# Kernel tuning notes

Measured on AMD Instinct MI355X. Metric: run time of the kernel, lower is better.

The kernel has to match this reference:

```python
import jax, jax.numpy as jnp
import numpy as np

EPS = 1e-12
SIMILARITY = 'dot'  # non-tensor forward arg, closed over


def setup_inputs() -> dict:
    key = jax.random.key(0)
    k1, k2, k3, k4 = jax.random.split(key, 4)
    N, M, D = 4096, 8192, 512
    x = jax.random.normal(k1, (N, D), dtype=jnp.float32)
    x_n = jax.random.normal(k2, (M, D), dtype=jnp.float32)
    # Linear(D, 3) params
    W = jax.random.normal(k3, (3, D), dtype=jnp.float32) * (1.0 / np.sqrt(D))
    bias = jax.random.normal(k4, (3,), dtype=jnp.float32) * 0.01
    return {"x": x, "x_n": x_n, "W": W, "bias": bias}


def _sim_matrix(x, x_n, similarity):
    if similarity == 'l2':
        d2 = (jnp.sum(x * x, 1)[:, None] - 2.0 * (x @ x_n.T)
              + jnp.sum(x_n * x_n, 1)[None, :])
        return -jnp.sqrt(jnp.maximum(d2, 0.0))
    elif similarity == 'l1':
        return -jnp.sum(jnp.abs(x[:, None, :] - x_n[None, :, :]), axis=-1)
    elif similarity == 'dot':
        return (x @ x_n.T) / x.shape[1]
    elif similarity == 'cos':
        xn = x / jnp.linalg.norm(x, axis=1, keepdims=True)
        yn = x_n / jnp.linalg.norm(x_n, axis=1, keepdims=True)
        return xn @ yn.T


def reference(x, x_n, W, bias):
    # pointwise params from a Linear(D,3)+Sigmoid head, clamped to (eps, 1-eps)
    p = jnp.clip(jax.nn.sigmoid(x @ W.T + bias), EPS, 1.0 - EPS)  # [N,3]
    a = p[:, 0:1]
    b = p[:, 1:2]
    s = p[:, 2:3]
    b = a + b * (1.0 - a)

    sim = _sim_matrix(x, x_n, SIMILARITY)                # [N,M]
    smin = jnp.min(sim, axis=1, keepdims=True)
    smax = jnp.max(sim, axis=1, keepdims=True)
    sim_norm = (sim - smin) / (smax - smin)

    # x != x_n -> plain row max (torch.equal branch is False)
    top_sims = jnp.max(sim_norm, axis=1, keepdims=True)  # [N,1]
    a = jnp.minimum(a, top_sims) - EPS

    num = jnp.maximum(jnp.abs(sim_norm - a) ** (1.0 / s), EPS)
    denom = num + jnp.maximum(jnp.abs(b - sim_norm) ** (1.0 / s), EPS)
    soft_mask = num / denom

    lo = sim_norm < a
    hi = sim_norm > b
    soft_mask = jnp.where(lo, 0.0, jnp.where(hi, 1.0, soft_mask))
    # safe log: masked-to-0 entries give -inf forward, zero grad (matches torch)
    safe = jnp.where(lo, 1.0, soft_mask)
    log_mask = jnp.where(lo, -jnp.inf, jnp.log(safe))
    return sim + log_mask
```

## Files before the change

### kernel.cpp

```cpp
#include <hip/hip_runtime.h>
#include <hip/hip_fp16.h>
#include <math.h>

#define EPSF 1e-12f
#define NEG_HUGE (-1e30f)

typedef _Float16 half8_t __attribute__((ext_vector_type(8)));
typedef _Float16 half4_t __attribute__((ext_vector_type(4)));
typedef float floatx4 __attribute__((ext_vector_type(4)));

__device__ __forceinline__ float sigmoid_stable(float v) {
    if (v >= 0.0f) {
        return 1.0f / (1.0f + expf(-v));
    } else {
        float e = expf(v);
        return e / (1.0f + e);
    }
}

__global__ __launch_bounds__(64) void row_params_kernel(
    const float* __restrict__ x, const float* __restrict__ W,
    const float* __restrict__ bias,
    float* __restrict__ aeff, float* __restrict__ bnew, float* __restrict__ tinv)
{
    const int r = blockIdx.x;
    const int l = threadIdx.x;
    const float* xr = x + (size_t)r * 512;
    float s0 = 0.0f, s1 = 0.0f, s2 = 0.0f;
#pragma unroll
    for (int i = 0; i < 8; ++i) {
        int e = l * 8 + i;
        float xv = xr[e];
        s0 = fmaf(xv, W[e], s0);
        s1 = fmaf(xv, W[512 + e], s1);
        s2 = fmaf(xv, W[1024 + e], s2);
    }
#pragma unroll
    for (int off = 32; off > 0; off >>= 1) {
        s0 += __shfl_xor(s0, off);
        s1 += __shfl_xor(s1, off);
        s2 += __shfl_xor(s2, off);
    }
    if (l == 0) {
        float p0 = fminf(fmaxf(sigmoid_stable(s0 + bias[0]), EPSF), 1.0f);
        float p1 = fminf(fmaxf(sigmoid_stable(s1 + bias[1]), EPSF), 1.0f);
        float p2 = fminf(fmaxf(sigmoid_stable(s2 + bias[2]), EPSF), 1.0f);
        float b = p0 + p1 * (1.0f - p0);
        float ae = fminf(p0, 1.0f) - EPSF;
        aeff[r] = ae;
        bnew[r] = b;
        tinv[r] = 1.0f / p2;
    }
}

__global__ __launch_bounds__(256) void split_fp32_f16_kernel(
    const float* __restrict__ src, _Float16* __restrict__ dst,
    int seg_lo, int nrows)
{
    int idx = blockIdx.x * 256 + threadIdx.x;
    int row = idx >> 7;
    int c = (idx & 127) << 2;
    if (row >= nrows) return;
    float4 v = *(const float4*)(src + (size_t)row * 512 + c);
    _Float16 h0 = (_Float16)v.x, h1 = (_Float16)v.y,
             h2 = (_Float16)v.z, h3 = (_Float16)v.w;
    half4_t hv = {h0, h1, h2, h3};
    half4_t lv = {(_Float16)(v.x - (float)h0), (_Float16)(v.y - (float)h1),
                  (_Float16)(v.z - (float)h2), (_Float16)(v.w - (float)h3)};
    _Float16* d = dst + (size_t)row * 1536 + c;
    *(half4_t*)(d) = hv;
    *(half4_t*)(d + 512)  = (seg_lo == 1) ? lv : hv;
    *(half4_t*)(d + 1024) = (seg_lo == 1) ? hv : lv;
}

__device__ __forceinline__ void load_tile_row16(
    const _Float16* gbase, _Float16* lds_base, int lane)
{
    const _Float16* g = gbase + (size_t)(lane >> 2) * 1536 + (size_t)(lane & 3) * 8;
    __builtin_amdgcn_global_load_lds(
        (const __attribute__((address_space(1))) unsigned int*)g,
        (__attribute__((address_space(3))) unsigned int*)lds_base,
        16, 0, 0);
}

__global__ __launch_bounds__(256) void mfma_gemm_kernel(
    const _Float16* __restrict__ A, const _Float16* __restrict__ B,
    float* __restrict__ C)
{
    constexpr int Kp = 1536;
    constexpr int N = 8192;
    __shared__ __align__(16) _Float16 As[128 * 32];
    __shared__ __align__(16) _Float16 Bs[128 * 32];

    const int t = threadIdx.x;
    const int wave = t >> 6;
    const int lane = t & 63;
    const int bx = blockIdx.x;
    const int by = blockIdx.y;

    const _Float16* Abase = A + (size_t)(by * 128 + wave * 16) * Kp;
    const _Float16* Bbase = B + (size_t)(bx * 128 + wave * 16) * Kp;
    _Float16* AsW0 = &As[(wave * 16) * 32];
    _Float16* AsW1 = &As[(64 + wave * 16) * 32];
    _Float16* BsW0 = &Bs[(wave * 16) * 32];
    _Float16* BsW1 = &Bs[(64 + wave * 16) * 32];
    const size_t rs64 = (size_t)64 * Kp;

    const int wm = (wave >> 1) * 64;
    const int wn = (wave & 1) * 64;
    const _Float16* aptr = &As[(wm + (lane & 15)) * 32 + (lane >> 4) * 8];
    const _Float16* bptr = &Bs[(wn + (lane & 15)) * 32 + (lane >> 4) * 8];

    floatx4 acc[4][4] = {};

    for (int kt = 0; kt < Kp / 32; ++kt) {
        const _Float16* Ak = Abase + kt * 32;
        const _Float16* Bk = Bbase + kt * 32;
        load_tile_row16(Ak, AsW0, lane);
        load_tile_row16(Ak + rs64, AsW1, lane);
        load_tile_row16(Bk, BsW0, lane);
        load_tile_row16(Bk + rs64, BsW1, lane);
        __syncthreads();

        half8_t af[4], bf[4];
#pragma unroll
        for (int i = 0; i < 4; ++i) af[i] = *(const half8_t*)(aptr + i * 16 * 32);
#pragma unroll
        for (int j = 0; j < 4; ++j) bf[j] = *(const half8_t*)(bptr + j * 16 * 32);
#pragma unroll
        for (int i = 0; i < 4; ++i)
#pragma unroll
            for (int j = 0; j < 4; ++j)
                acc[i][j] = __builtin_amdgcn_mfma_f32_16x16x32_f16(
                    af[i], bf[j], acc[i][j], 0, 0, 0);
        __syncthreads();
    }

    const float sc = 1.0f / 512.0f;
    const int row0 = by * 128 + wm + (lane >> 4) * 4;
    const int col0 = bx * 128 + wn + (lane & 15);
#pragma unroll
    for (int i = 0; i < 4; ++i) {
#pragma unroll
        for (int r = 0; r < 4; ++r) {
            float* cp = C + (size_t)(row0 + i * 16 + r) * N + col0;
#pragma unroll
            for (int j = 0; j < 4; ++j)
                cp[j * 16] = acc[i][j][r] * sc;
        }
    }
}

#define BM 128
#define BN 128
#define BK 16
__global__ __launch_bounds__(256) void sgemm_nt_kernel(
    const float* __restrict__ A, const float* __restrict__ B,
    float* __restrict__ C)
{
    const int K = 512;
    const int N = 8192;
    __shared__ float As[BK][BM];
    __shared__ float Bs[BK][BN];
    const int t = threadIdx.x;
    const int bx = blockIdx.x, by = blockIdx.y;
    const int m0 = t >> 2;
    const int kq = (t & 3) << 2;
    const float* Ap = A + ((size_t)(by * BM + m0) * K + kq);
    const float* Bp = B + ((size_t)(bx * BN + m0) * K + kq);
    const int tx = t & 15, ty = t >> 4;
    float acc[8][8] = {};
    float4 a0 = *(const float4*)(Ap), a1 = *(const float4*)(Ap + (size_t)64 * K);
    float4 b0 = *(const float4*)(Bp), b1 = *(const float4*)(Bp + (size_t)64 * K);
    for (int kt = 0; kt < K / BK; ++kt) {
        As[kq + 0][m0] = a0.x; As[kq + 1][m0] = a0.y; As[kq + 2][m0] = a0.z; As[kq + 3][m0] = a0.w;
        As[kq + 0][m0 + 64] = a1.x; As[kq + 1][m0 + 64] = a1.y; As[kq + 2][m0 + 64] = a1.z; As[kq + 3][m0 + 64] = a1.w;
        Bs[kq + 0][m0] = b0.x; Bs[kq + 1][m0] = b0.y; Bs[kq + 2][m0] = b0.z; Bs[kq + 3][m0] = b0.w;
        Bs[kq + 0][m0 + 64] = b1.x; Bs[kq + 1][m0 + 64] = b1.y; Bs[kq + 2][m0 + 64] = b1.z; Bs[kq + 3][m0 + 64] = b1.w;
        __syncthreads();
        if (kt + 1 < K / BK) {
            const float* Ap2 = Ap + (size_t)(kt + 1) * BK;
            const float* Bp2 = Bp + (size_t)(kt + 1) * BK;
            a0 = *(const float4*)(Ap2); a1 = *(const float4*)(Ap2 + (size_t)64 * K);
            b0 = *(const float4*)(Bp2); b1 = *(const float4*)(Bp2 + (size_t)64 * K);
        }
#pragma unroll
        for (int k = 0; k < BK; ++k) {
            float4 xa0 = *(const float4*)(&As[k][ty * 8]);
            float4 xa1 = *(const float4*)(&As[k][ty * 8 + 4]);
            float4 yb0 = *(const float4*)(&Bs[k][tx * 8]);
            float4 yb1 = *(const float4*)(&Bs[k][tx * 8 + 4]);
            float av[8] = {xa0.x, xa0.y, xa0.z, xa0.w, xa1.x, xa1.y, xa1.z, xa1.w};
            float bv[8] = {yb0.x, yb0.y, yb0.z, yb0.w, yb1.x, yb1.y, yb1.z, yb1.w};
#pragma unroll
            for (int i = 0; i < 8; ++i)
#pragma unroll
                for (int j = 0; j < 8; ++j)
                    acc[i][j] = fmaf(av[i], bv[j], acc[i][j]);
        }
        __syncthreads();
    }
    const float sc = 1.0f / 512.0f;
    const int gm = by * BM + ty * 8, gn = bx * BN + tx * 8;
#pragma unroll
    for (int i = 0; i < 8; ++i) {
        float4 o0 = make_float4(acc[i][0] * sc, acc[i][1] * sc, acc[i][2] * sc, acc[i][3] * sc);
        float4 o1 = make_float4(acc[i][4] * sc, acc[i][5] * sc, acc[i][6] * sc, acc[i][7] * sc);
        float* cp = C + (size_t)(gm + i) * N + gn;
        *(float4*)(cp) = o0;
        *(float4*)(cp + 4) = o1;
    }
}

__global__ __launch_bounds__(256) void row_minmax_kernel(
    const float* __restrict__ C, float* __restrict__ smin, float* __restrict__ smax)
{
    const int r = blockIdx.x;
    const float4* row = (const float4*)(C + (size_t)r * 8192);
    float mn = INFINITY, mx = -INFINITY;
#pragma unroll
    for (int i = 0; i < 8; ++i) {
        float4 v = row[threadIdx.x + i * 256];
        mn = fminf(mn, fminf(fminf(v.x, v.y), fminf(v.z, v.w)));
        mx = fmaxf(mx, fmaxf(fmaxf(v.x, v.y), fmaxf(v.z, v.w)));
    }
#pragma unroll
    for (int off = 32; off > 0; off >>= 1) {
        mn = fminf(mn, __shfl_xor(mn, off));
        mx = fmaxf(mx, __shfl_xor(mx, off));
    }
    __shared__ float smn[4], smx[4];
    if ((threadIdx.x & 63) == 0) {
        smn[threadIdx.x >> 6] = mn;
        smx[threadIdx.x >> 6] = mx;
    }
    __syncthreads();
    if (threadIdx.x == 0) {
        mn = fminf(fminf(smn[0], smn[1]), fminf(smn[2], smn[3]));
        mx = fmaxf(fmaxf(smx[0], smx[1]), fmaxf(smx[2], smx[3]));
        smin[r] = mn;
        smax[r] = mx;
    }
}

__device__ __forceinline__ float fast_pow(float x, float t) {
    return __expf(t * __logf(x));
}

__global__ __launch_bounds__(256) void epilogue_kernel(
    float* __restrict__ C,
    const float* __restrict__ aeff, const float* __restrict__ bnew,
    const float* __restrict__ tinv,
    const float* __restrict__ smin, const float* __restrict__ smax)
{
    const int r = blockIdx.y;
    const int c4 = blockIdx.x * 256 + threadIdx.x;
    const float a = aeff[r];
    const float b = bnew[r];
    const float t = tinv[r];
    const float mn = smin[r];
    const float range = smax[r] - mn;
    const float inv_range = (range > 0.0f) ? (1.0f / range) : 0.0f;

    float4* p = (float4*)(C + (size_t)r * 8192) + c4;
    float4 v = *p;
    float sv[4] = {v.x, v.y, v.z, v.w};
    float out[4];
#pragma unroll
    for (int i = 0; i < 4; ++i) {
        float sim = sv[i];
        float sn = (sim - mn) * inv_range;
        float lm;
        if (sn < a) {
            lm = NEG_HUGE;
        } else if (sn > b) {
            lm = 0.0f;
        } else {
            float num = fmaxf(fast_pow(fabsf(sn - a), t), EPSF);
            float den = num + fmaxf(fast_pow(fabsf(b - sn), t), EPSF);
            lm = __logf(num / den);
        }
        out[i] = sim + lm;
    }
    *p = make_float4(out[0], out[1], out[2], out[3]);
}

extern "C" void kernel_launch(void* const* d_in, const int* in_sizes, int n_in,
                              void* d_out, int out_size, void* d_ws, size_t ws_size,
                              hipStream_t stream)
{
    const float* x    = (const float*)d_in[0];
    const float* x_n  = (const float*)d_in[1];
    const float* W    = (const float*)d_in[2];
    const float* bias = (const float*)d_in[3];
    float* C = (float*)d_out;
    float* ws = (float*)d_ws;

    float* aeff = ws;
    float* bnew = ws + 4096;
    float* tinv = ws + 8192;
    float* smin = ws + 12288;
    float* smax = ws + 16384;

    const size_t a2_off = 128 * 1024;
    const size_t a2_bytes = (size_t)4096 * 1536 * 2;
    const size_t b2_off = a2_off + a2_bytes;
    const size_t need = b2_off + (size_t)8192 * 1536 * 2;

    row_params_kernel<<<4096, 64, 0, stream>>>(x, W, bias, aeff, bnew, tinv);

    if (ws_size >= need) {
        _Float16* A2 = (_Float16*)((char*)d_ws + a2_off);
        _Float16* B2 = (_Float16*)((char*)d_ws + b2_off);
        split_fp32_f16_kernel<<<2048, 256, 0, stream>>>(x, A2, 2, 4096);
        split_fp32_f16_kernel<<<4096, 256, 0, stream>>>(x_n, B2, 1, 8192);
        mfma_gemm_kernel<<<dim3(64, 32), 256, 0, stream>>>(A2, B2, C);
    } else {
        sgemm_nt_kernel<<<dim3(8192 / BN, 4096 / BM), 256, 0, stream>>>(x, x_n, C);
    }

    row_minmax_kernel<<<4096, 256, 0, stream>>>(C, smin, smax);
    epilogue_kernel<<<dim3(8192 / 4 / 256, 4096), 256, 0, stream>>>(C, aeff, bnew, tinv, smin, smax);
}
```

Baseline: 336.3 us.

## Fuse row min/max into GEMM epilogue via ordered-int atomics; merge split kernels

The separate row min/max pass over the 128MB similarity matrix is removed. Each GEMM block instead reduces its tile's per-row min and max with shuffles, then updates global ordered-uint encodings using atomicMin and atomicMax, which row_params_kernel initializes. The two fp16 split kernels become one launch, the epilogue uses nontemporal loads and stores, and the fp32 SGEMM fallback is dropped, so the workspace is assumed large enough. This saves a full read of C and two launches, at the cost of atomic contention and extra epilogue work inside the GEMM.

```diff
diff --git a/kernel.cpp b/kernel.cpp
--- a/kernel.cpp
+++ b/kernel.cpp
@@ -18,10 +18,20 @@
     }
 }
 
+__device__ __forceinline__ unsigned enc_ord(float f) {
+    unsigned u = __float_as_uint(f);
+    return (u & 0x80000000u) ? ~u : (u | 0x80000000u);
+}
+__device__ __forceinline__ float dec_ord(unsigned e) {
+    unsigned u = (e & 0x80000000u) ? (e & 0x7fffffffu) : ~e;
+    return __uint_as_float(u);
+}
+
 __global__ __launch_bounds__(64) void row_params_kernel(
     const float* __restrict__ x, const float* __restrict__ W,
     const float* __restrict__ bias,
-    float* __restrict__ aeff, float* __restrict__ bnew, float* __restrict__ tinv)
+    float* __restrict__ aeff, float* __restrict__ bnew, float* __restrict__ tinv,
+    unsigned* __restrict__ encMin, unsigned* __restrict__ encMax)
 {
     const int r = blockIdx.x;
     const int l = threadIdx.x;
@@ -50,27 +60,40 @@
         aeff[r] = ae;
         bnew[r] = b;
         tinv[r] = 1.0f / p2;
-    }
-}
-
-__global__ __launch_bounds__(256) void split_fp32_f16_kernel(
-    const float* __restrict__ src, _Float16* __restrict__ dst,
-    int seg_lo, int nrows)
+        encMin[r] = 0xFFFFFFFFu;
+        encMax[r] = 0u;
+    }
+}
+
+__global__ __launch_bounds__(256) void split_both_kernel(
+    const float* __restrict__ x, const float* __restrict__ xn,
+    _Float16* __restrict__ A2, _Float16* __restrict__ B2)
 {
     int idx = blockIdx.x * 256 + threadIdx.x;
     int row = idx >> 7;
     int c = (idx & 127) << 2;
-    if (row >= nrows) return;
-    float4 v = *(const float4*)(src + (size_t)row * 512 + c);
+    const float* src;
+    _Float16* dst;
+    bool isB;
+    if (row < 4096) {
+        src = x + (size_t)row * 512 + c;
+        dst = A2 + (size_t)row * 1536 + c;
+        isB = false;
+    } else {
+        int r = row - 4096;
+        src = xn + (size_t)r * 512 + c;
+        dst = B2 + (size_t)r * 1536 + c;
+        isB = true;
+    }
+    float4 v = *(const float4*)src;
     _Float16 h0 = (_Float16)v.x, h1 = (_Float16)v.y,
              h2 = (_Float16)v.z, h3 = (_Float16)v.w;
     half4_t hv = {h0, h1, h2, h3};
     half4_t lv = {(_Float16)(v.x - (float)h0), (_Float16)(v.y - (float)h1),
                   (_Float16)(v.z - (float)h2), (_Float16)(v.w - (float)h3)};
-    _Float16* d = dst + (size_t)row * 1536 + c;
-    *(half4_t*)(d) = hv;
-    *(half4_t*)(d + 512)  = (seg_lo == 1) ? lv : hv;
-    *(half4_t*)(d + 1024) = (seg_lo == 1) ? hv : lv;
+    *(half4_t*)(dst) = hv;
+    *(half4_t*)(dst + 512)  = isB ? lv : hv;
+    *(half4_t*)(dst + 1024) = isB ? hv : lv;
 }
 
 __device__ __forceinline__ void load_tile_row16(
@@ -85,7 +108,8 @@
 
 __global__ __launch_bounds__(256) void mfma_gemm_kernel(
     const _Float16* __restrict__ A, const _Float16* __restrict__ B,
-    float* __restrict__ C)
+    float* __restrict__ C,
+    unsigned* __restrict__ encMin, unsigned* __restrict__ encMax)
 {
     constexpr int Kp = 1536;
     constexpr int N = 8192;
@@ -149,97 +173,37 @@
                 cp[j * 16] = acc[i][j][r] * sc;
         }
     }
-}
-
-#define BM 128
-#define BN 128
-#define BK 16
-__global__ __launch_bounds__(256) void sgemm_nt_kernel(
-    const float* __restrict__ A, const float* __restrict__ B,
-    float* __restrict__ C)
-{
-    const int K = 512;
-    const int N = 8192;
-    __shared__ float As[BK][BM];
-    __shared__ float Bs[BK][BN];
-    const int t = threadIdx.x;
-    const int bx = blockIdx.x, by = blockIdx.y;
-    const int m0 = t >> 2;
-    const int kq = (t & 3) << 2;
-    const float* Ap = A + ((size_t)(by * BM + m0) * K + kq);
-    const float* Bp = B + ((size_t)(bx * BN + m0) * K + kq);
-    const int tx = t & 15, ty = t >> 4;
-    float acc[8][8] = {};
-    float4 a0 = *(const float4*)(Ap), a1 = *(const float4*)(Ap + (size_t)64 * K);
-    float4 b0 = *(const float4*)(Bp), b1 = *(const float4*)(Bp + (size_t)64 * K);
-    for (int kt = 0; kt < K / BK; ++kt) {
-        As[kq + 0][m0] = a0.x; As[kq + 1][m0] = a0.y; As[kq + 2][m0] = a0.z; As[kq + 3][m0] = a0.w;
-        As[kq + 0][m0 + 64] = a1.x; As[kq + 1][m0 + 64] = a1.y; As[kq + 2][m0 + 64] = a1.z; As[kq + 3][m0 + 64] = a1.w;
-        Bs[kq + 0][m0] = b0.x; Bs[kq + 1][m0] = b0.y; Bs[kq + 2][m0] = b0.z; Bs[kq + 3][m0] = b0.w;
-        Bs[kq + 0][m0 + 64] = b1.x; Bs[kq + 1][m0 + 64] = b1.y; Bs[kq + 2][m0 + 64] = b1.z; Bs[kq + 3][m0 + 64] = b1.w;
-        __syncthreads();
-        if (kt + 1 < K / BK) {
-            const float* Ap2 = Ap + (size_t)(kt + 1) * BK;
-            const float* Bp2 = Bp + (size_t)(kt + 1) * BK;
-            a0 = *(const float4*)(Ap2); a1 = *(const float4*)(Ap2 + (size_t)64 * K);
-            b0 = *(const float4*)(Bp2); b1 = *(const float4*)(Bp2 + (size_t)64 * K);
+
+    float mnv[4][4], mxv[4][4];
+#pragma unroll
+    for (int i = 0; i < 4; ++i)
+#pragma unroll
+        for (int r = 0; r < 4; ++r) {
+            float lo = fminf(fminf(acc[i][0][r], acc[i][1][r]),
+                             fminf(acc[i][2][r], acc[i][3][r]));
+            float hi = fmaxf(fmaxf(acc[i][0][r], acc[i][1][r]),
+                             fmaxf(acc[i][2][r], acc[i][3][r]));
+            mnv[i][r] = lo * sc;
+            mxv[i][r] = hi * sc;
         }
 #pragma unroll
-        for (int k = 0; k < BK; ++k) {
-            float4 xa0 = *(const float4*)(&As[k][ty * 8]);
-            float4 xa1 = *(const float4*)(&As[k][ty * 8 + 4]);
-            float4 yb0 = *(const float4*)(&Bs[k][tx * 8]);
-            float4 yb1 = *(const float4*)(&Bs[k][tx * 8 + 4]);
-            float av[8] = {xa0.x, xa0.y, xa0.z, xa0.w, xa1.x, xa1.y, xa1.z, xa1.w};
-            float bv[8] = {yb0.x, yb0.y, yb0.z, yb0.w, yb1.x, yb1.y, yb1.z, yb1.w};
-#pragma unroll
-            for (int i = 0; i < 8; ++i)
-#pragma unroll
-                for (int j = 0; j < 8; ++j)
-                    acc[i][j] = fmaf(av[i], bv[j], acc[i][j]);
-        }
-        __syncthreads();
-    }
-    const float sc = 1.0f / 512.0f;
-    const int gm = by * BM + ty * 8, gn = bx * BN + tx * 8;
-#pragma unroll
-    for (int i = 0; i < 8; ++i) {
-        float4 o0 = make_float4(acc[i][0] * sc, acc[i][1] * sc, acc[i][2] * sc, acc[i][3] * sc);
-        float4 o1 = make_float4(acc[i][4] * sc, acc[i][5] * sc, acc[i][6] * sc, acc[i][7] * sc);
-        float* cp = C + (size_t)(gm + i) * N + gn;
-        *(float4*)(cp) = o0;
-        *(float4*)(cp + 4) = o1;
-    }
-}
-
-__global__ __launch_bounds__(256) void row_minmax_kernel(
-    const float* __restrict__ C, float* __restrict__ smin, float* __restrict__ smax)
-{
-    const int r = blockIdx.x;
-    const float4* row = (const float4*)(C + (size_t)r * 8192);
-    float mn = INFINITY, mx = -INFINITY;
-#pragma unroll
-    for (int i = 0; i < 8; ++i) {
-        float4 v = row[threadIdx.x + i * 256];
-        mn = fminf(mn, fminf(fminf(v.x, v.y), fminf(v.z, v.w)));
-        mx = fmaxf(mx, fmaxf(fmaxf(v.x, v.y), fmaxf(v.z, v.w)));
-    }
-#pragma unroll
-    for (int off = 32; off > 0; off >>= 1) {
-        mn = fminf(mn, __shfl_xor(mn, off));
-        mx = fmaxf(mx, __shfl_xor(mx, off));
-    }
-    __shared__ float smn[4], smx[4];
-    if ((threadIdx.x & 63) == 0) {
-        smn[threadIdx.x >> 6] = mn;
-        smx[threadIdx.x >> 6] = mx;
-    }
-    __syncthreads();
-    if (threadIdx.x == 0) {
-        mn = fminf(fminf(smn[0], smn[1]), fminf(smn[2], smn[3]));
-        mx = fmaxf(fmaxf(smx[0], smx[1]), fmaxf(smx[2], smx[3]));
-        smin[r] = mn;
-        smax[r] = mx;
+    for (int off = 1; off < 16; off <<= 1)
+#pragma unroll
+        for (int i = 0; i < 4; ++i)
+#pragma unroll
+            for (int r = 0; r < 4; ++r) {
+                mnv[i][r] = fminf(mnv[i][r], __shfl_xor(mnv[i][r], off));
+                mxv[i][r] = fmaxf(mxv[i][r], __shfl_xor(mxv[i][r], off));
+            }
+    if ((lane & 15) == 0) {
+#pragma unroll
+        for (int i = 0; i < 4; ++i)
+#pragma unroll
+            for (int r = 0; r < 4; ++r) {
+                int row = row0 + i * 16 + r;
+                atomicMin(&encMin[row], enc_ord(mnv[i][r]));
+                atomicMax(&encMax[row], enc_ord(mxv[i][r]));
+            }
     }
 }
 
@@ -251,24 +215,23 @@
     float* __restrict__ C,
     const float* __restrict__ aeff, const float* __restrict__ bnew,
     const float* __restrict__ tinv,
-    const float* __restrict__ smin, const float* __restrict__ smax)
+    const unsigned* __restrict__ encMin, const unsigned* __restrict__ encMax)
 {
     const int r = blockIdx.y;
     const int c4 = blockIdx.x * 256 + threadIdx.x;
     const float a = aeff[r];
     const float b = bnew[r];
     const float t = tinv[r];
-    const float mn = smin[r];
-    const float range = smax[r] - mn;
+    const float mn = dec_ord(encMin[r]);
+    const float range = dec_ord(encMax[r]) - mn;
     const float inv_range = (range > 0.0f) ? (1.0f / range) : 0.0f;
 
-    float4* p = (float4*)(C + (size_t)r * 8192) + c4;
-    float4 v = *p;
-    float sv[4] = {v.x, v.y, v.z, v.w};
-    float out[4];
+    floatx4* p = (floatx4*)(C + (size_t)r * 8192) + c4;
+    floatx4 v = __builtin_nontemporal_load(p);
+    floatx4 out;
 #pragma unroll
     for (int i = 0; i < 4; ++i) {
-        float sim = sv[i];
+        float sim = v[i];
         float sn = (sim - mn) * inv_range;
         float lm;
         if (sn < a) {
@@ -282,7 +245,7 @@
         }
         out[i] = sim + lm;
     }
-    *p = make_float4(out[0], out[1], out[2], out[3]);
+    __builtin_nontemporal_store(out, p);
 }
 
 extern "C" void kernel_launch(void* const* d_in, const int* in_sizes, int n_in,
@@ -299,26 +262,19 @@
     float* aeff = ws;
     float* bnew = ws + 4096;
     float* tinv = ws + 8192;
-    float* smin = ws + 12288;
-    float* smax = ws + 16384;
+    unsigned* encMin = (unsigned*)(ws + 12288);
+    unsigned* encMax = (unsigned*)(ws + 16384);
 
     const size_t a2_off = 128 * 1024;
     const size_t a2_bytes = (size_t)4096 * 1536 * 2;
     const size_t b2_off = a2_off + a2_bytes;
-    const size_t need = b2_off + (size_t)8192 * 1536 * 2;
-
-    row_params_kernel<<<4096, 64, 0, stream>>>(x, W, bias, aeff, bnew, tinv);
-
-    if (ws_size >= need) {
-        _Float16* A2 = (_Float16*)((char*)d_ws + a2_off);
-        _Float16* B2 = (_Float16*)((char*)d_ws + b2_off);
-        split_fp32_f16_kernel<<<2048, 256, 0, stream>>>(x, A2, 2, 4096);
-        split_fp32_f16_kernel<<<4096, 256, 0, stream>>>(x_n, B2, 1, 8192);
-        mfma_gemm_kernel<<<dim3(64, 32), 256, 0, stream>>>(A2, B2, C);
-    } else {
-        sgemm_nt_kernel<<<dim3(8192 / BN, 4096 / BM), 256, 0, stream>>>(x, x_n, C);
-    }
-
-    row_minmax_kernel<<<4096, 256, 0, stream>>>(C, smin, smax);
-    epilogue_kernel<<<dim3(8192 / 4 / 256, 4096), 256, 0, stream>>>(C, aeff, bnew, tinv, smin, smax);
-}
+    _Float16* A2 = (_Float16*)((char*)d_ws + a2_off);
+    _Float16* B2 = (_Float16*)((char*)d_ws + b2_off);
+
+    row_params_kernel<<<4096, 64, 0, stream>>>(x, W, bias, aeff, bnew, tinv,
+                                               encMin, encMax);
+    split_both_kernel<<<6144, 256, 0, stream>>>(x, x_n, A2, B2);
+    mfma_gemm_kernel<<<dim3(64, 32), 256, 0, stream>>>(A2, B2, C, encMin, encMax);
+    epilogue_kernel<<<dim3(8, 4096), 256, 0, stream>>>(C, aeff, bnew, tinv,
+                                                       encMin, encMax);
+}
```

New measurement: 342.0 us. No clear change (+1.7%).

## Fuse row min/max partials into MFMA GEMM epilogue and merge split kernels

Applied to the files above, without the earlier changes.

The GEMM epilogue now computes per-row min/max partials over each wave's 64-column slice and writes them to a workspace buffer. A small reduction kernel combines them, which removes the full-matrix row_minmax pass that re-read the 128MB similarity matrix. The two fp16 split kernels are merged into a single launch, and the epilogue uses nontemporal loads and stores. The cost is extra shuffle work and partial-buffer writes inside the GEMM, plus a larger workspace requirement.

```diff
diff --git a/kernel.cpp b/kernel.cpp
--- a/kernel.cpp
+++ b/kernel.cpp
@@ -53,24 +53,35 @@
     }
 }
 
-__global__ __launch_bounds__(256) void split_fp32_f16_kernel(
-    const float* __restrict__ src, _Float16* __restrict__ dst,
-    int seg_lo, int nrows)
+__global__ __launch_bounds__(256) void split_both_kernel(
+    const float* __restrict__ x, const float* __restrict__ xn,
+    _Float16* __restrict__ A2, _Float16* __restrict__ B2)
 {
     int idx = blockIdx.x * 256 + threadIdx.x;
     int row = idx >> 7;
     int c = (idx & 127) << 2;
-    if (row >= nrows) return;
-    float4 v = *(const float4*)(src + (size_t)row * 512 + c);
+    const float* src;
+    _Float16* dst;
+    bool isB;
+    if (row < 4096) {
+        src = x + (size_t)row * 512 + c;
+        dst = A2 + (size_t)row * 1536 + c;
+        isB = false;
+    } else {
+        int r = row - 4096;
+        src = xn + (size_t)r * 512 + c;
+        dst = B2 + (size_t)r * 1536 + c;
+        isB = true;
+    }
+    float4 v = *(const float4*)src;
     _Float16 h0 = (_Float16)v.x, h1 = (_Float16)v.y,
              h2 = (_Float16)v.z, h3 = (_Float16)v.w;
     half4_t hv = {h0, h1, h2, h3};
     half4_t lv = {(_Float16)(v.x - (float)h0), (_Float16)(v.y - (float)h1),
                   (_Float16)(v.z - (float)h2), (_Float16)(v.w - (float)h3)};
-    _Float16* d = dst + (size_t)row * 1536 + c;
-    *(half4_t*)(d) = hv;
-    *(half4_t*)(d + 512)  = (seg_lo == 1) ? lv : hv;
-    *(half4_t*)(d + 1024) = (seg_lo == 1) ? hv : lv;
+    *(half4_t*)(dst) = hv;
+    *(half4_t*)(dst + 512)  = isB ? lv : hv;
+    *(half4_t*)(dst + 1024) = isB ? hv : lv;
 }
 
 __device__ __forceinline__ void load_tile_row16(
@@ -85,7 +96,8 @@
 
 __global__ __launch_bounds__(256) void mfma_gemm_kernel(
     const _Float16* __restrict__ A, const _Float16* __restrict__ B,
-    float* __restrict__ C)
+    float* __restrict__ C,
+    float* __restrict__ pmin, float* __restrict__ pmax)
 {
     constexpr int Kp = 1536;
     constexpr int N = 8192;
@@ -148,6 +160,60 @@
             for (int j = 0; j < 4; ++j)
                 cp[j * 16] = acc[i][j][r] * sc;
         }
+    }
+
+    float mnv[4][4], mxv[4][4];
+#pragma unroll
+    for (int i = 0; i < 4; ++i)
+#pragma unroll
+        for (int r = 0; r < 4; ++r) {
+            float lo = fminf(fminf(acc[i][0][r], acc[i][1][r]),
+                             fminf(acc[i][2][r], acc[i][3][r]));
+            float hi = fmaxf(fmaxf(acc[i][0][r], acc[i][1][r]),
+                             fmaxf(acc[i][2][r], acc[i][3][r]));
+            mnv[i][r] = lo * sc;
+            mxv[i][r] = hi * sc;
+        }
+#pragma unroll
+    for (int off = 1; off < 16; off <<= 1)
+#pragma unroll
+        for (int i = 0; i < 4; ++i)
+#pragma unroll
+            for (int r = 0; r < 4; ++r) {
+                mnv[i][r] = fminf(mnv[i][r], __shfl_xor(mnv[i][r], off));
+                mxv[i][r] = fmaxf(mxv[i][r], __shfl_xor(mxv[i][r], off));
+            }
+    if ((lane & 15) == 0) {
+        const int pb = bx * 2 + (wave & 1);
+#pragma unroll
+        for (int i = 0; i < 4; ++i)
+#pragma unroll
+            for (int r = 0; r < 4; ++r) {
+                size_t row = (size_t)(row0 + i * 16 + r);
+                pmin[(row << 7) + pb] = mnv[i][r];
+                pmax[(row << 7) + pb] = mxv[i][r];
+            }
+    }
+}
+
+__global__ __launch_bounds__(64) void minmax_reduce_kernel(
+    const float* __restrict__ pmin, const float* __restrict__ pmax,
+    float* __restrict__ smin, float* __restrict__ smax)
+{
+    const int r = blockIdx.x;
+    const int l = threadIdx.x;
+    const float* bmin = pmin + ((size_t)r << 7);
+    const float* bmax = pmax + ((size_t)r << 7);
+    float mn = fminf(bmin[l], bmin[l + 64]);
+    float mx = fmaxf(bmax[l], bmax[l + 64]);
+#pragma unroll
+    for (int off = 32; off > 0; off >>= 1) {
+        mn = fminf(mn, __shfl_xor(mn, off));
+        mx = fmaxf(mx, __shfl_xor(mx, off));
+    }
+    if (l == 0) {
+        smin[r] = mn;
+        smax[r] = mx;
     }
 }
 
@@ -262,13 +328,12 @@
     const float range = smax[r] - mn;
     const float inv_range = (range > 0.0f) ? (1.0f / range) : 0.0f;
 
-    float4* p = (float4*)(C + (size_t)r * 8192) + c4;
-    float4 v = *p;
-    float sv[4] = {v.x, v.y, v.z, v.w};
-    float out[4];
+    floatx4* p = (floatx4*)(C + (size_t)r * 8192) + c4;
+    floatx4 v = __builtin_nontemporal_load(p);
+    floatx4 out;
 #pragma unroll
     for (int i = 0; i < 4; ++i) {
-        float sim = sv[i];
+        float sim = v[i];
         float sn = (sim - mn) * inv_range;
         float lm;
         if (sn < a) {
@@ -282,7 +347,7 @@
         }
         out[i] = sim + lm;
     }
-    *p = make_float4(out[0], out[1], out[2], out[3]);
+    __builtin_nontemporal_store(out, p);
 }
 
 extern "C" void kernel_launch(void* const* d_in, const int* in_sizes, int n_in,
@@ -302,7 +367,9 @@
     float* smin = ws + 12288;
     float* smax = ws + 16384;
 
-    const size_t a2_off = 128 * 1024;
+    const size_t pmin_off = 128 * 1024;
+    const size_t pbytes = (size_t)4096 * 128 * 4;
+    const size_t a2_off = pmin_off + 2 * pbytes;
     const size_t a2_bytes = (size_t)4096 * 1536 * 2;
     const size_t b2_off = a2_off + a2_bytes;
     const size_t need = b2_off + (size_t)8192 * 1536 * 2;
@@ -310,15 +377,18 @@
     row_params_kernel<<<4096, 64, 0, stream>>>(x, W, bias, aeff, bnew, tinv);
 
     if (ws_size >= need) {
+        float* pmin = (float*)((char*)d_ws + pmin_off);
+        float* pmax = (float*)((char*)d_ws + pmin_off + pbytes);
         _Float16* A2 = (_Float16*)((char*)d_ws + a2_off);
         _Float16* B2 = (_Float16*)((char*)d_ws + b2_off);
-        split_fp32_f16_kernel<<<2048, 256, 0, stream>>>(x, A2, 2, 4096);
-        split_fp32_f16_kernel<<<4096, 256, 0, stream>>>(x_n, B2, 1, 8192);
-        mfma_gemm_kernel<<<dim3(64, 32), 256, 0, stream>>>(A2, B2, C);
+        split_both_kernel<<<6144, 256, 0, stream>>>(x, x_n, A2, B2);
+        mfma_gemm_kernel<<<dim3(64, 32), 256, 0, stream>>>(A2, B2, C, pmin, pmax);
+        minmax_reduce_kernel<<<4096, 64, 0, stream>>>(pmin, pmax, smin, smax);
     } else {
         sgemm_nt_kernel<<<dim3(8192 / BN, 4096 / BM), 256, 0, stream>>>(x, x_n, C);
-    }
-
-    row_minmax_kernel<<<4096, 256, 0, stream>>>(C, smin, smax);
-    epilogue_kernel<<<dim3(8192 / 4 / 256, 4096), 256, 0, stream>>>(C, aeff, bnew, tinv, smin, smax);
-}
+        row_minmax_kernel<<<4096, 256, 0, stream>>>(C, smin, smax);
+    }
+
+    epilogue_kernel<<<dim3(8, 4096), 256, 0, stream>>>(C, aeff, bnew, tinv,
+                                                       smin, smax);
+}
```

Result: faster. 326.5 us (-2.9%).
